# Kernel tuning notes

Hardware: AMD Instinct MI355X
Metric: run time of the kernel (lower is better)

## Reference

```python
import jax, jax.numpy as jnp
import numpy as np

N_NODES = 100000
N_EDGES = 1600000
D_IN = 64
D_OUT = 64
K_ORDERS = 4  # K+1 Chebyshev orders (K=3)


def setup_inputs() -> dict:
    key = jax.random.key(0)
    k1, k2, k3, k4, k5 = jax.random.split(key, 5)
    x = jax.random.normal(k1, (N_NODES, D_IN), dtype=jnp.float32)
    edge_index = jax.random.randint(k2, (2, N_EDGES), 0, N_NODES, dtype=jnp.int64)
    edge_attr = jax.random.uniform(k3, (N_EDGES,), dtype=jnp.float32)
    weight = jax.random.normal(k4, (K_ORDERS, D_IN, D_OUT), dtype=jnp.float32) * 0.05
    bias = jax.random.normal(k5, (D_OUT,), dtype=jnp.float32) * 0.05
    return {"x": x, "edge_index": edge_index, "edge_attr": edge_attr,
            "weight": weight, "bias": bias}


def reference(x, edge_index, edge_attr, weight, bias):
    n = x.shape[0]
    row, col = edge_index[0], edge_index[1]
    # degree = number of edges per destination node (row)
    deg = jax.ops.segment_sum(jnp.ones_like(edge_attr), row, num_segments=n)
    dinv = jnp.where(deg > 0, deg ** -0.5, 0.0)
    # negative normalized adjacency acting as rescaled Laplacian
    lap = -dinv[row] * edge_attr * dinv[col]  # [E]

    def spmm(h):  # out[row] += lap * h[col]
        return jax.ops.segment_sum(lap[:, None] * h[col], row, num_segments=n)

    k_orders = weight.shape[0]
    tx0 = x
    out = tx0 @ weight[0]
    tx1 = spmm(tx0)
    out = out + tx1 @ weight[1]
    for k in range(2, k_orders):  # small fixed K, fine to unroll
        tx2 = 2.0 * spmm(tx1) - tx0
        out = out + tx2 @ weight[k]
        tx0, tx1 = tx1, tx2
    return out + bias
```

## Files before the change

### kernel.cpp

```cpp
#include <hip/hip_runtime.h>

#define D 64
#define BLK 256

#define NBSHIFT 9
#define NODES_PER_BKT 512
#define TA 4096

typedef unsigned int uint32;
typedef __attribute__((ext_vector_type(8))) short bf16x8;
typedef __attribute__((ext_vector_type(4))) float f32x4;

__device__ inline uint32 f2bf_u(float f) {
    uint32 u = __float_as_uint(f);
    u += 0x7FFFu + ((u >> 16) & 1u);
    return u >> 16;
}

__global__ void cvt_kernel(const float* __restrict__ x, uint2* __restrict__ xb, int n4) {
    int i = blockIdx.x * BLK + threadIdx.x;
    if (i < n4) {
        float4 v = ((const float4*)x)[i];
        uint2 pack;
        pack.x = f2bf_u(v.x) | (f2bf_u(v.y) << 16);
        pack.y = f2bf_u(v.z) | (f2bf_u(v.w) << 16);
        xb[i] = pack;
    }
}

__global__ void wf_kernel(const float* __restrict__ W, uint4* __restrict__ Wf) {
    int tid = blockIdx.x * 256 + threadIdx.x;
    int l = tid & 63;
    int g = tid >> 6;
    int kh = g & 1;
    int t = (g >> 1) & 3;
    int w = g >> 3;
    int n = t * 16 + (l & 15);
    int kbase = kh * 32 + (l >> 4) * 8;
    uint32 pk[4];
    #pragma unroll
    for (int i = 0; i < 4; ++i) {
        uint32 b0 = f2bf_u(W[(size_t)w * 4096 + (size_t)(kbase + 2 * i) * 64 + n]);
        uint32 b1 = f2bf_u(W[(size_t)w * 4096 + (size_t)(kbase + 2 * i + 1) * 64 + n]);
        pk[i] = b0 | (b1 << 16);
    }
    Wf[tid] = make_uint4(pk[0], pk[1], pk[2], pk[3]);
}

__global__ void hist_kernel(const int* __restrict__ row, uint32* __restrict__ bcount, int E) {
    __shared__ uint32 h[256];
    int tid = threadIdx.x;
    h[tid] = 0;
    __syncthreads();
    int base = blockIdx.x * TA;
    int end = min(base + TA, E);
    for (int e = base + tid; e < end; e += 256)
        atomicAdd(&h[(uint32)row[e] >> NBSHIFT], 1u);
    __syncthreads();
    if (h[tid]) atomicAdd(&bcount[tid], h[tid]);
}

__global__ void scan256_kernel(const uint32* __restrict__ bcount, uint32* __restrict__ gcursor,
                               uint32* __restrict__ bbase, int E) {
    __shared__ uint32 s[256];
    int tid = threadIdx.x;
    uint32 v = bcount[tid];
    s[tid] = v;
    __syncthreads();
    for (int off = 1; off < 256; off <<= 1) {
        uint32 t = (tid >= off) ? s[tid - off] : 0u;
        __syncthreads();
        s[tid] += t;
        __syncthreads();
    }
    uint32 excl = s[tid] - v;
    gcursor[tid] = excl;
    bbase[tid] = excl;
    if (tid == 255) bbase[256] = (uint32)E;
}

__global__ void binA_kernel(const int* __restrict__ row, const int* __restrict__ col,
                            const float* __restrict__ attr,
                            uint32* __restrict__ gcursor, int2* __restrict__ binned, int E) {
    __shared__ uint32 hist[256], baseg[256], lstart[256], lcur[256];
    __shared__ int2 stage[TA];
    __shared__ unsigned char sbkt[TA];
    int tid = threadIdx.x;
    int tile = blockIdx.x * TA;
    hist[tid] = 0;
    __syncthreads();

    uint32 px[16], py[16], bk[16];
    #pragma unroll
    for (int k = 0; k < 16; ++k) {
        int e = tile + k * 256 + tid;
        bk[k] = 0xFFFFFFFFu;
        if (e < E) {
            int r = row[e], c = col[e];
            uint32 b = (uint32)r >> NBSHIFT;
            bk[k] = b;
            px[k] = ((uint32)(r & (NODES_PER_BKT - 1)) << 17) | (uint32)c;
            py[k] = __float_as_uint(attr[e]);
            atomicAdd(&hist[b], 1u);
        }
    }
    __syncthreads();
    lcur[tid] = hist[tid];
    __syncthreads();
    for (int off = 1; off < 256; off <<= 1) {
        uint32 t = (tid >= off) ? lcur[tid - off] : 0u;
        __syncthreads();
        lcur[tid] += t;
        __syncthreads();
    }
    lstart[tid] = lcur[tid] - hist[tid];
    if (hist[tid] > 0) baseg[tid] = atomicAdd(&gcursor[tid], hist[tid]);
    lcur[tid] = lstart[tid];
    __syncthreads();
    #pragma unroll
    for (int k = 0; k < 16; ++k) {
        if (bk[k] != 0xFFFFFFFFu) {
            uint32 pos = atomicAdd(&lcur[bk[k]], 1u);
            stage[pos] = make_int2((int)px[k], (int)py[k]);
            sbkt[pos] = (unsigned char)bk[k];
        }
    }
    __syncthreads();
    int cnt = min(TA, E - tile);
    for (int i = tid; i < cnt; i += 256) {
        uint32 b = sbkt[i];
        uint32 dst = baseg[b] + (uint32)i - lstart[b];
        binned[dst] = stage[i];
    }
}

__global__ void binBdeg_kernel(const int2* __restrict__ binned, const uint32* __restrict__ bbase,
                               uint32* __restrict__ rowptr, float* __restrict__ dinv,
                               int N, int E) {
    __shared__ uint32 cnt[NODES_PER_BKT];
    __shared__ uint32 ps[256];
    int b = blockIdx.x;
    int tid = threadIdx.x;
    cnt[tid] = 0;
    cnt[tid + 256] = 0;
    __syncthreads();
    uint32 start = bbase[b], end = bbase[b + 1];
    for (uint32 i = start + tid; i < end; i += 256)
        atomicAdd(&cnt[(uint32)binned[i].x >> 17], 1u);
    __syncthreads();
    uint32 c0 = cnt[2 * tid], c1 = cnt[2 * tid + 1];
    ps[tid] = c0 + c1;
    __syncthreads();
    for (int off = 1; off < 256; off <<= 1) {
        uint32 t = (tid >= off) ? ps[tid - off] : 0u;
        __syncthreads();
        ps[tid] += t;
        __syncthreads();
    }
    uint32 pexcl = ps[tid] - (c0 + c1);
    int base = b << NBSHIFT;
    int n0 = base + 2 * tid, n1 = n0 + 1;
    if (n0 < N) {
        rowptr[n0] = start + pexcl;
        dinv[n0] = c0 ? rsqrtf((float)c0) : 0.0f;
    }
    if (n1 < N) {
        rowptr[n1] = start + pexcl + c0;
        dinv[n1] = c1 ? rsqrtf((float)c1) : 0.0f;
    }
    if (b == gridDim.x - 1 && tid == 0) rowptr[N] = (uint32)E;
}

__global__ void binBsort_kernel(const int2* __restrict__ binned, const uint32* __restrict__ bbase,
                                const uint32* __restrict__ rowptr, const float* __restrict__ dinv,
                                int2* __restrict__ pairs, int N) {
    __shared__ uint32 lcur[NODES_PER_BKT];
    __shared__ float ldin[NODES_PER_BKT];
    int b = blockIdx.x;
    int tid = threadIdx.x;
    int base = b << NBSHIFT;
    uint32 start = bbase[b], end = bbase[b + 1];
    for (int t = tid; t < NODES_PER_BKT; t += 256) {
        int node = base + t;
        lcur[t] = (node < N) ? (rowptr[node] - start) : 0u;
        ldin[t] = (node < N) ? dinv[node] : 0.0f;
    }
    __syncthreads();
    for (uint32 i = start + tid; i < end; i += 256) {
        int2 rec = binned[i];
        uint32 x = (uint32)rec.x;
        uint32 rl = x >> 17;
        uint32 c = x & 0x1FFFFu;
        float lap = -ldin[rl] * __int_as_float(rec.y) * dinv[c];
        uint32 pos = atomicAdd(&lcur[rl], 1u);
        pairs[start + pos] = make_int2((int)(c << 7), __float_as_int(lap));
    }
}

#define LOAD16(J, END, ESAFE, M0, M1, H0, H1)                          \
    {                                                                  \
        uint32 i0_ = (J) + q, i1_ = (J) + 8 + q;                       \
        uint32 c0_ = (i0_ < (END)) ? i0_ : (ESAFE);                    \
        uint32 c1_ = (i1_ < (END)) ? i1_ : (ESAFE);                    \
        M0 = pairs[c0_];                                               \
        M1 = pairs[c1_];                                               \
        H0 = *(const uint4*)(hb + (uint32)M0.x + off);                 \
        H1 = *(const uint4*)(hb + (uint32)M1.x + off);                 \
    }

#define FMA16(J, END, M0, M1, H0, H1, A)                               \
    {                                                                  \
        uint32 i0_ = (J) + q, i1_ = (J) + 8 + q;                       \
        float l0_ = (i0_ < (END)) ? __int_as_float(M0.y) : 0.0f;       \
        float l1_ = (i1_ < (END)) ? __int_as_float(M1.y) : 0.0f;       \
        A[0] += l0_ * __uint_as_float(H0.x << 16);                     \
        A[1] += l0_ * __uint_as_float(H0.x & 0xFFFF0000u);             \
        A[2] += l0_ * __uint_as_float(H0.y << 16);                     \
        A[3] += l0_ * __uint_as_float(H0.y & 0xFFFF0000u);             \
        A[4] += l0_ * __uint_as_float(H0.z << 16);                     \
        A[5] += l0_ * __uint_as_float(H0.z & 0xFFFF0000u);             \
        A[6] += l0_ * __uint_as_float(H0.w << 16);                     \
        A[7] += l0_ * __uint_as_float(H0.w & 0xFFFF0000u);             \
        A[0] += l1_ * __uint_as_float(H1.x << 16);                     \
        A[1] += l1_ * __uint_as_float(H1.x & 0xFFFF0000u);             \
        A[2] += l1_ * __uint_as_float(H1.y << 16);                     \
        A[3] += l1_ * __uint_as_float(H1.y & 0xFFFF0000u);             \
        A[4] += l1_ * __uint_as_float(H1.z << 16);                     \
        A[5] += l1_ * __uint_as_float(H1.z & 0xFFFF0000u);             \
        A[6] += l1_ * __uint_as_float(H1.w << 16);                     \
        A[7] += l1_ * __uint_as_float(H1.w & 0xFFFF0000u);             \
    }

__global__ void spmm2r_kernel(const uint32* __restrict__ rowptr, const int2* __restrict__ pairs,
                              const char* __restrict__ hb, const uint4* __restrict__ prev,
                              uint4* __restrict__ out, float scale, int N) {
    int wid = blockIdx.x * 4 + (threadIdx.x >> 6);
    int nA = wid * 2;
    if (nA >= N) return;
    int lane = threadIdx.x & 63;
    int q = lane >> 3;
    int sub = lane & 7;
    int off = sub * 16;
    bool hasB = (nA + 1 < N);

    uint2 rpA = *(const uint2*)(rowptr + nA);
    uint32 eBr = hasB ? rowptr[nA + 2] : rpA.y;
    uint32 jA   = __builtin_amdgcn_readfirstlane(rpA.x);
    uint32 endA = __builtin_amdgcn_readfirstlane(rpA.y);
    uint32 jB   = endA;
    uint32 endB = __builtin_amdgcn_readfirstlane(eBr);
    uint32 esA = (endA > jA) ? endA - 1 : 0u;
    uint32 esB = (endB > jB) ? endB - 1 : 0u;

    int nq = nA + (q & 1);
    uint4 pv = make_uint4(0u, 0u, 0u, 0u);
    if (prev && q < 2 && nq < N) pv = prev[(size_t)nq * 8 + sub];

    float aA[8], aB[8];
    #pragma unroll
    for (int i = 0; i < 8; ++i) { aA[i] = 0.0f; aB[i] = 0.0f; }

    int2 mA0, mA1, mA2, mA3, mB0, mB1, mB2, mB3;
    uint4 hA0, hA1, hA2, hA3, hB0, hB1, hB2, hB3;

    bool dA = (jA + 16 < endA);
    bool dB = (jB + 16 < endB);

    LOAD16(jA, endA, esA, mA0, mA1, hA0, hA1);
    LOAD16(jB, endB, esB, mB0, mB1, hB0, hB1);
    if (dA) LOAD16(jA + 16, endA, esA, mA2, mA3, hA2, hA3);
    if (dB) LOAD16(jB + 16, endB, esB, mB2, mB3, hB2, hB3);
    FMA16(jA, endA, mA0, mA1, hA0, hA1, aA);
    FMA16(jB, endB, mB0, mB1, hB0, hB1, aB);
    if (dA) FMA16(jA + 16, endA, mA2, mA3, hA2, hA3, aA);
    if (dB) FMA16(jB + 16, endB, mB2, mB3, hB2, hB3, aB);
    jA += 32;
    jB += 32;

    while (jA < endA) {
        LOAD16(jA, endA, esA, mA0, mA1, hA0, hA1);
        FMA16(jA, endA, mA0, mA1, hA0, hA1, aA);
        if (jA + 16 < endA) {
            LOAD16(jA + 16, endA, esA, mA2, mA3, hA2, hA3);
            FMA16(jA + 16, endA, mA2, mA3, hA2, hA3, aA);
        }
        jA += 32;
    }
    while (jB < endB) {
        LOAD16(jB, endB, esB, mB0, mB1, hB0, hB1);
        FMA16(jB, endB, mB0, mB1, hB0, hB1, aB);
        if (jB + 16 < endB) {
            LOAD16(jB + 16, endB, esB, mB2, mB3, hB2, hB3);
            FMA16(jB + 16, endB, mB2, mB3, hB2, hB3, aB);
        }
        jB += 32;
    }

    #pragma unroll
    for (int i = 0; i < 8; ++i) {
        aA[i] += __shfl_xor(aA[i], 8);
        aA[i] += __shfl_xor(aA[i], 16);
        aA[i] += __shfl_xor(aA[i], 32);
        aB[i] += __shfl_xor(aB[i], 8);
        aB[i] += __shfl_xor(aB[i], 16);
        aB[i] += __shfl_xor(aB[i], 32);
    }

    if (q < 2 && nq < N) {
        bool isB = (q == 1);
        float r[8];
        #pragma unroll
        for (int i = 0; i < 8; ++i) r[i] = scale * (isB ? aB[i] : aA[i]);
        if (prev) {
            r[0] -= __uint_as_float(pv.x << 16);
            r[1] -= __uint_as_float(pv.x & 0xFFFF0000u);
            r[2] -= __uint_as_float(pv.y << 16);
            r[3] -= __uint_as_float(pv.y & 0xFFFF0000u);
            r[4] -= __uint_as_float(pv.z << 16);
            r[5] -= __uint_as_float(pv.z & 0xFFFF0000u);
            r[6] -= __uint_as_float(pv.w << 16);
            r[7] -= __uint_as_float(pv.w & 0xFFFF0000u);
        }
        uint4 pack;
        pack.x = f2bf_u(r[0]) | (f2bf_u(r[1]) << 16);
        pack.y = f2bf_u(r[2]) | (f2bf_u(r[3]) << 16);
        pack.z = f2bf_u(r[4]) | (f2bf_u(r[5]) << 16);
        pack.w = f2bf_u(r[6]) | (f2bf_u(r[7]) << 16);
        out[(size_t)nq * 8 + sub] = pack;
    }
}

__global__ void gemm_mfma(const uint4* __restrict__ h0, const uint4* __restrict__ h1,
                          const uint4* __restrict__ h2, const uint4* __restrict__ h3,
                          const uint4* __restrict__ Wf, const float* __restrict__ bias,
                          float* __restrict__ out, int N) {
    int tid = threadIdx.x;
    int wave = tid >> 6;
    int lane = tid & 63;
    int quad = lane >> 4;
    int lo = lane & 15;
    int m0 = blockIdx.x * 64 + wave * 16;
    int mrow = m0 + lo;
    int mclamp = min(mrow, N - 1);

    f32x4 acc[4] = {{0.f,0.f,0.f,0.f},{0.f,0.f,0.f,0.f},{0.f,0.f,0.f,0.f},{0.f,0.f,0.f,0.f}};
    const uint4* hs[4] = { h0, h1, h2, h3 };
    #pragma unroll
    for (int w = 0; w < 4; ++w) {
        union { uint4 u; bf16x8 v; } a0, a1;
        a0.u = hs[w][(size_t)mclamp * 8 + quad];
        a1.u = hs[w][(size_t)mclamp * 8 + 4 + quad];
        #pragma unroll
        for (int t = 0; t < 4; ++t) {
            union { uint4 u; bf16x8 v; } b0, b1;
            b0.u = Wf[(w * 8 + t * 2 + 0) * 64 + lane];
            b1.u = Wf[(w * 8 + t * 2 + 1) * 64 + lane];
            acc[t] = __builtin_amdgcn_mfma_f32_16x16x32_bf16(a0.v, b0.v, acc[t], 0, 0, 0);
            acc[t] = __builtin_amdgcn_mfma_f32_16x16x32_bf16(a1.v, b1.v, acc[t], 0, 0, 0);
        }
    }
    #pragma unroll
    for (int t = 0; t < 4; ++t) {
        int col = t * 16 + lo;
        float bv = bias[col];
        #pragma unroll
        for (int r = 0; r < 4; ++r) {
            int rowi = m0 + quad * 4 + r;
            if (rowi < N) out[(size_t)rowi * 64 + col] = acc[t][r] + bv;
        }
    }
}

extern "C" void kernel_launch(void* const* d_in, const int* in_sizes, int n_in,
                              void* d_out, int out_size, void* d_ws, size_t ws_size,
                              hipStream_t stream) {
    const float* x    = (const float*)d_in[0];
    const int*   ei   = (const int*)d_in[1];
    const float* attr = (const float*)d_in[2];
    const float* W    = (const float*)d_in[3];
    const float* bias = (const float*)d_in[4];
    float* out = (float*)d_out;

    const int N = in_sizes[0] / D;
    const int E = in_sizes[1] / 2;
    const int* row = ei;
    const int* col = ei + E;
    const int NB = (N + NODES_PER_BKT - 1) >> NBSHIFT;

    char* p = (char*)d_ws;
    int2*     pairs   = (int2*)p;                p += (size_t)E * 8;
    uint2*    xb      = (uint2*)p;               p += (size_t)N * D * 2;
    uint2*    T1      = (uint2*)p;               p += (size_t)N * D * 2;
    uint2*    T2      = (uint2*)p;               p += (size_t)N * D * 2;
    uint2*    T3      = (uint2*)p;               p += (size_t)N * D * 2;
    uint4*    Wf      = (uint4*)p;               p += 2048 * 16;
    uint32*   rowptr  = (uint32*)p;              p += (size_t)(N + 1) * 4;
    uint32*   bcount  = (uint32*)p;              p += 256 * 4;
    uint32*   gcursor = (uint32*)p;              p += 256 * 4;
    uint32*   bbase   = (uint32*)p;              p += 257 * 4;
    float*    dinv    = (float*)p;
    int2*     binned  = (int2*)T3;

    const int gSp = (N + 7) / 8;
    const int gGm = (N + 63) / 64;
    const int gTile = (E + TA - 1) / TA;
    const int gCvt = ((N * D / 4) + BLK - 1) / BLK;

    hipMemsetAsync(bcount, 0, 256 * 4, stream);
    cvt_kernel<<<gCvt, BLK, 0, stream>>>(x, xb, N * D / 4);
    wf_kernel<<<8, 256, 0, stream>>>(W, Wf);
    hist_kernel<<<gTile, 256, 0, stream>>>(row, bcount, E);
    scan256_kernel<<<1, 256, 0, stream>>>(bcount, gcursor, bbase, E);
    binA_kernel<<<gTile, 256, 0, stream>>>(row, col, attr, gcursor, binned, E);
    binBdeg_kernel<<<NB, 256, 0, stream>>>(binned, bbase, rowptr, dinv, N, E);
    binBsort_kernel<<<NB, 256, 0, stream>>>(binned, bbase, rowptr, dinv, pairs, N);

    spmm2r_kernel<<<gSp, BLK, 0, stream>>>(rowptr, pairs, (const char*)xb, nullptr, (uint4*)T1, 1.0f, N);
    spmm2r_kernel<<<gSp, BLK, 0, stream>>>(rowptr, pairs, (const char*)T1, (const uint4*)xb, (uint4*)T2, 2.0f, N);
    spmm2r_kernel<<<gSp, BLK, 0, stream>>>(rowptr, pairs, (const char*)T2, (const uint4*)T1, (uint4*)T3, 2.0f, N);
    gemm_mfma<<<gGm, BLK, 0, stream>>>((const uint4*)xb, (const uint4*)T1, (const uint4*)T2,
                                       (const uint4*)T3, Wf, bias, out, N);
}
```

Baseline: 291.6 us.

## Split SpMM feature dimension into four column chunks across blocks

```diff
diff --git a/kernel.cpp b/kernel.cpp
--- a/kernel.cpp
+++ b/kernel.cpp
@@ -197,50 +197,42 @@
     }
 }
 
-#define LOAD16(J, END, ESAFE, M0, M1, H0, H1)                          \
-    {                                                                  \
-        uint32 i0_ = (J) + q, i1_ = (J) + 8 + q;                       \
-        uint32 c0_ = (i0_ < (END)) ? i0_ : (ESAFE);                    \
-        uint32 c1_ = (i1_ < (END)) ? i1_ : (ESAFE);                    \
-        M0 = pairs[c0_];                                               \
-        M1 = pairs[c1_];                                               \
-        H0 = *(const uint4*)(hb + (uint32)M0.x + off);                 \
-        H1 = *(const uint4*)(hb + (uint32)M1.x + off);                 \
-    }
-
-#define FMA16(J, END, M0, M1, H0, H1, A)                               \
-    {                                                                  \
-        uint32 i0_ = (J) + q, i1_ = (J) + 8 + q;                       \
-        float l0_ = (i0_ < (END)) ? __int_as_float(M0.y) : 0.0f;       \
-        float l1_ = (i1_ < (END)) ? __int_as_float(M1.y) : 0.0f;       \
-        A[0] += l0_ * __uint_as_float(H0.x << 16);                     \
-        A[1] += l0_ * __uint_as_float(H0.x & 0xFFFF0000u);             \
-        A[2] += l0_ * __uint_as_float(H0.y << 16);                     \
-        A[3] += l0_ * __uint_as_float(H0.y & 0xFFFF0000u);             \
-        A[4] += l0_ * __uint_as_float(H0.z << 16);                     \
-        A[5] += l0_ * __uint_as_float(H0.z & 0xFFFF0000u);             \
-        A[6] += l0_ * __uint_as_float(H0.w << 16);                     \
-        A[7] += l0_ * __uint_as_float(H0.w & 0xFFFF0000u);             \
-        A[0] += l1_ * __uint_as_float(H1.x << 16);                     \
-        A[1] += l1_ * __uint_as_float(H1.x & 0xFFFF0000u);             \
-        A[2] += l1_ * __uint_as_float(H1.y << 16);                     \
-        A[3] += l1_ * __uint_as_float(H1.y & 0xFFFF0000u);             \
-        A[4] += l1_ * __uint_as_float(H1.z << 16);                     \
-        A[5] += l1_ * __uint_as_float(H1.z & 0xFFFF0000u);             \
-        A[6] += l1_ * __uint_as_float(H1.w << 16);                     \
-        A[7] += l1_ * __uint_as_float(H1.w & 0xFFFF0000u);             \
-    }
-
-__global__ void spmm2r_kernel(const uint32* __restrict__ rowptr, const int2* __restrict__ pairs,
-                              const char* __restrict__ hb, const uint4* __restrict__ prev,
-                              uint4* __restrict__ out, float scale, int N) {
-    int wid = blockIdx.x * 4 + (threadIdx.x >> 6);
+#define LOAD16C(J, END, ESAFE, X0, L0, X1, L1, H0, H1)                          \
+    {                                                                           \
+        uint32 i0_ = (J) + q, i1_ = (J) + 8 + q;                                \
+        uint32 c0_ = (i0_ < (END)) ? i0_ : (ESAFE);                             \
+        uint32 c1_ = (i1_ < (END)) ? i1_ : (ESAFE);                             \
+        unsigned long long p0_ = __builtin_nontemporal_load(pairs64 + c0_);     \
+        unsigned long long p1_ = __builtin_nontemporal_load(pairs64 + c1_);     \
+        X0 = (uint32)p0_;                                                       \
+        X1 = (uint32)p1_;                                                       \
+        L0 = (i0_ < (END)) ? __uint_as_float((uint32)(p0_ >> 32)) : 0.0f;       \
+        L1 = (i1_ < (END)) ? __uint_as_float((uint32)(p1_ >> 32)) : 0.0f;       \
+        H0 = *(const uint32*)(hb + X0 + coff);                                  \
+        H1 = *(const uint32*)(hb + X1 + coff);                                  \
+    }
+
+#define FMA16C(L0, L1, H0, H1, A)                                               \
+    {                                                                           \
+        A[0] += L0 * __uint_as_float(H0 << 16);                                 \
+        A[1] += L0 * __uint_as_float(H0 & 0xFFFF0000u);                         \
+        A[0] += L1 * __uint_as_float(H1 << 16);                                 \
+        A[1] += L1 * __uint_as_float(H1 & 0xFFFF0000u);                         \
+    }
+
+__global__ void spmm2rc_kernel(const uint32* __restrict__ rowptr, const int2* __restrict__ pairs,
+                               const char* __restrict__ hb, const uint32* __restrict__ prev,
+                               uint32* __restrict__ out, float scale, int N) {
+    int chunk = blockIdx.x & 3;
+    int rg = blockIdx.x >> 2;
+    int wid = rg * 4 + (threadIdx.x >> 6);
     int nA = wid * 2;
     if (nA >= N) return;
     int lane = threadIdx.x & 63;
     int q = lane >> 3;
     int sub = lane & 7;
-    int off = sub * 16;
+    int coff = chunk * 32 + sub * 4;
+    const unsigned long long* pairs64 = (const unsigned long long*)pairs;
     bool hasB = (nA + 1 < N);
 
     uint2 rpA = *(const uint2*)(rowptr + nA);
@@ -253,51 +245,50 @@
     uint32 esB = (endB > jB) ? endB - 1 : 0u;
 
     int nq = nA + (q & 1);
-    uint4 pv = make_uint4(0u, 0u, 0u, 0u);
-    if (prev && q < 2 && nq < N) pv = prev[(size_t)nq * 8 + sub];
-
-    float aA[8], aB[8];
-    #pragma unroll
-    for (int i = 0; i < 8; ++i) { aA[i] = 0.0f; aB[i] = 0.0f; }
-
-    int2 mA0, mA1, mA2, mA3, mB0, mB1, mB2, mB3;
-    uint4 hA0, hA1, hA2, hA3, hB0, hB1, hB2, hB3;
+    uint32 pv = 0u;
+    if (prev && q < 2 && nq < N)
+        pv = __builtin_nontemporal_load(prev + (size_t)nq * 32 + chunk * 8 + sub);
+
+    float aA[2] = {0.0f, 0.0f}, aB[2] = {0.0f, 0.0f};
+    uint32 xA0, xA1, xA2, xA3, xB0, xB1, xB2, xB3;
+    float lA0, lA1, lA2, lA3, lB0, lB1, lB2, lB3;
+    uint32 hA0, hA1, hA2, hA3, hB0, hB1, hB2, hB3;
 
     bool dA = (jA + 16 < endA);
     bool dB = (jB + 16 < endB);
 
-    LOAD16(jA, endA, esA, mA0, mA1, hA0, hA1);
-    LOAD16(jB, endB, esB, mB0, mB1, hB0, hB1);
-    if (dA) LOAD16(jA + 16, endA, esA, mA2, mA3, hA2, hA3);
-    if (dB) LOAD16(jB + 16, endB, esB, mB2, mB3, hB2, hB3);
-    FMA16(jA, endA, mA0, mA1, hA0, hA1, aA);
-    FMA16(jB, endB, mB0, mB1, hB0, hB1, aB);
-    if (dA) FMA16(jA + 16, endA, mA2, mA3, hA2, hA3, aA);
-    if (dB) FMA16(jB + 16, endB, mB2, mB3, hB2, hB3, aB);
+    LOAD16C(jA, endA, esA, xA0, lA0, xA1, lA1, hA0, hA1);
+    LOAD16C(jB, endB, esB, xB0, lB0, xB1, lB1, hB0, hB1);
+    if (dA) LOAD16C(jA + 16, endA, esA, xA2, lA2, xA3, lA3, hA2, hA3);
+    if (dB) LOAD16C(jB + 16, endB, esB, xB2, lB2, xB3, lB3, hB2, hB3);
+    FMA16C(lA0, lA1, hA0, hA1, aA);
+    FMA16C(lB0, lB1, hB0, hB1, aB);
+    if (dA) FMA16C(lA2, lA3, hA2, hA3, aA);
+    if (dB) FMA16C(lB2, lB3, hB2, hB3, aB);
     jA += 32;
     jB += 32;
 
     while (jA < endA) {
-        LOAD16(jA, endA, esA, mA0, mA1, hA0, hA1);
-        FMA16(jA, endA, mA0, mA1, hA0, hA1, aA);
+        LOAD16C(jA, endA, esA, xA0, lA0, xA1, lA1, hA0, hA1);
+        FMA16C(lA0, lA1, hA0, hA1, aA);
         if (jA + 16 < endA) {
-            LOAD16(jA + 16, endA, esA, mA2, mA3, hA2, hA3);
-            FMA16(jA + 16, endA, mA2, mA3, hA2, hA3, aA);
+            LOAD16C(jA + 16, endA, esA, xA2, lA2, xA3, lA3, hA2, hA3);
+            FMA16C(lA2, lA3, hA2, hA3, aA);
         }
         jA += 32;
     }
     while (jB < endB) {
-        LOAD16(jB, endB, esB, mB0, mB1, hB0, hB1);
-        FMA16(jB, endB, mB0, mB1, hB0, hB1, aB);
+        LOAD16C(jB, endB, esB, xB0, lB0, xB1, lB1, hB0, hB1);
+        FMA16C(lB0, lB1, hB0, hB1, aB);
         if (jB + 16 < endB) {
-            LOAD16(jB + 16, endB, esB, mB2, mB3, hB2, hB3);
-            FMA16(jB + 16, endB, mB2, mB3, hB2, hB3, aB);
+            LOAD16C(jB + 16, endB, esB, xB2, lB2, xB3, lB3, hB2, hB3);
+            FMA16C(lB2, lB3, hB2, hB3, aB);
         }
         jB += 32;
     }
 
     #pragma unroll
-    for (int i = 0; i < 8; ++i) {
+    for (int i = 0; i < 2; ++i) {
         aA[i] += __shfl_xor(aA[i], 8);
         aA[i] += __shfl_xor(aA[i], 16);
         aA[i] += __shfl_xor(aA[i], 32);
@@ -308,25 +299,13 @@
 
     if (q < 2 && nq < N) {
         bool isB = (q == 1);
-        float r[8];
-        #pragma unroll
-        for (int i = 0; i < 8; ++i) r[i] = scale * (isB ? aB[i] : aA[i]);
+        float r0 = scale * (isB ? aB[0] : aA[0]);
+        float r1 = scale * (isB ? aB[1] : aA[1]);
         if (prev) {
-            r[0] -= __uint_as_float(pv.x << 16);
-            r[1] -= __uint_as_float(pv.x & 0xFFFF0000u);
-            r[2] -= __uint_as_float(pv.y << 16);
-            r[3] -= __uint_as_float(pv.y & 0xFFFF0000u);
-            r[4] -= __uint_as_float(pv.z << 16);
-            r[5] -= __uint_as_float(pv.z & 0xFFFF0000u);
-            r[6] -= __uint_as_float(pv.w << 16);
-            r[7] -= __uint_as_float(pv.w & 0xFFFF0000u);
-        }
-        uint4 pack;
-        pack.x = f2bf_u(r[0]) | (f2bf_u(r[1]) << 16);
-        pack.y = f2bf_u(r[2]) | (f2bf_u(r[3]) << 16);
-        pack.z = f2bf_u(r[4]) | (f2bf_u(r[5]) << 16);
-        pack.w = f2bf_u(r[6]) | (f2bf_u(r[7]) << 16);
-        out[(size_t)nq * 8 + sub] = pack;
+            r0 -= __uint_as_float(pv << 16);
+            r1 -= __uint_as_float(pv & 0xFFFF0000u);
+        }
+        out[(size_t)nq * 32 + chunk * 8 + sub] = f2bf_u(r0) | (f2bf_u(r1) << 16);
     }
 }
 
@@ -401,7 +380,7 @@
     float*    dinv    = (float*)p;
     int2*     binned  = (int2*)T3;
 
-    const int gSp = (N + 7) / 8;
+    const int gSpC = ((N + 7) / 8) * 4;
     const int gGm = (N + 63) / 64;
     const int gTile = (E + TA - 1) / TA;
     const int gCvt = ((N * D / 4) + BLK - 1) / BLK;
@@ -415,9 +394,9 @@
     binBdeg_kernel<<<NB, 256, 0, stream>>>(binned, bbase, rowptr, dinv, N, E);
     binBsort_kernel<<<NB, 256, 0, stream>>>(binned, bbase, rowptr, dinv, pairs, N);
 
-    spmm2r_kernel<<<gSp, BLK, 0, stream>>>(rowptr, pairs, (const char*)xb, nullptr, (uint4*)T1, 1.0f, N);
-    spmm2r_kernel<<<gSp, BLK, 0, stream>>>(rowptr, pairs, (const char*)T1, (const uint4*)xb, (uint4*)T2, 2.0f, N);
-    spmm2r_kernel<<<gSp, BLK, 0, stream>>>(rowptr, pairs, (const char*)T2, (const uint4*)T1, (uint4*)T3, 2.0f, N);
+    spmm2rc_kernel<<<gSpC, BLK, 0, stream>>>(rowptr, pairs, (const char*)xb, nullptr, (uint32*)T1, 1.0f, N);
+    spmm2rc_kernel<<<gSpC, BLK, 0, stream>>>(rowptr, pairs, (const char*)T1, (const uint32*)xb, (uint32*)T2, 2.0f, N);
+    spmm2rc_kernel<<<gSpC, BLK, 0, stream>>>(rowptr, pairs, (const char*)T2, (const uint32*)T1, (uint32*)T3, 2.0f, N);
     gemm_mfma<<<gGm, BLK, 0, stream>>>((const uint4*)xb, (const uint4*)T1, (const uint4*)T2,
                                        (const uint4*)T3, Wf, bias, out, N);
 }
```

New measurement: 524.1 us. +79.7%, slower.

## Fuse preprocessing kernels and merge binning passes with cooperative grid sync

Applied to the files above, without the earlier changes.

```diff
diff --git a/kernel.cpp b/kernel.cpp
--- a/kernel.cpp
+++ b/kernel.cpp
@@ -1,4 +1,7 @@
 #include <hip/hip_runtime.h>
+#include <hip/hip_cooperative_groups.h>
+
+namespace cg = cooperative_groups;
 
 #define D 64
 #define BLK 256
@@ -17,70 +20,74 @@
     return u >> 16;
 }
 
-__global__ void cvt_kernel(const float* __restrict__ x, uint2* __restrict__ xb, int n4) {
-    int i = blockIdx.x * BLK + threadIdx.x;
-    if (i < n4) {
-        float4 v = ((const float4*)x)[i];
-        uint2 pack;
-        pack.x = f2bf_u(v.x) | (f2bf_u(v.y) << 16);
-        pack.y = f2bf_u(v.z) | (f2bf_u(v.w) << 16);
-        xb[i] = pack;
-    }
-}
-
-__global__ void wf_kernel(const float* __restrict__ W, uint4* __restrict__ Wf) {
-    int tid = blockIdx.x * 256 + threadIdx.x;
-    int l = tid & 63;
-    int g = tid >> 6;
-    int kh = g & 1;
-    int t = (g >> 1) & 3;
-    int w = g >> 3;
-    int n = t * 16 + (l & 15);
-    int kbase = kh * 32 + (l >> 4) * 8;
-    uint32 pk[4];
-    #pragma unroll
-    for (int i = 0; i < 4; ++i) {
-        uint32 b0 = f2bf_u(W[(size_t)w * 4096 + (size_t)(kbase + 2 * i) * 64 + n]);
-        uint32 b1 = f2bf_u(W[(size_t)w * 4096 + (size_t)(kbase + 2 * i + 1) * 64 + n]);
-        pk[i] = b0 | (b1 << 16);
-    }
-    Wf[tid] = make_uint4(pk[0], pk[1], pk[2], pk[3]);
-}
-
-__global__ void hist_kernel(const int* __restrict__ row, uint32* __restrict__ bcount, int E) {
+__global__ void pre_kernel(const float* __restrict__ x, uint2* __restrict__ xb, int n4,
+                           const float* __restrict__ W, uint4* __restrict__ Wf,
+                           const int* __restrict__ row, uint32* __restrict__ bcount,
+                           uint32* __restrict__ ticket, uint32* __restrict__ bbase,
+                           int E, int gCvt, int gHist) {
+    int bid = blockIdx.x;
+    if (bid < gCvt) {
+        int i = bid * BLK + threadIdx.x;
+        if (i < n4) {
+            float4 v = ((const float4*)x)[i];
+            uint2 pack;
+            pack.x = f2bf_u(v.x) | (f2bf_u(v.y) << 16);
+            pack.y = f2bf_u(v.z) | (f2bf_u(v.w) << 16);
+            xb[i] = pack;
+        }
+        return;
+    }
+    if (bid < gCvt + 8) {
+        int tid = (bid - gCvt) * 256 + threadIdx.x;
+        int l = tid & 63;
+        int g = tid >> 6;
+        int kh = g & 1;
+        int t = (g >> 1) & 3;
+        int w = g >> 3;
+        int n = t * 16 + (l & 15);
+        int kbase = kh * 32 + (l >> 4) * 8;
+        uint32 pk[4];
+        #pragma unroll
+        for (int i = 0; i < 4; ++i) {
+            uint32 b0 = f2bf_u(W[(size_t)w * 4096 + (size_t)(kbase + 2 * i) * 64 + n]);
+            uint32 b1 = f2bf_u(W[(size_t)w * 4096 + (size_t)(kbase + 2 * i + 1) * 64 + n]);
+            pk[i] = b0 | (b1 << 16);
+        }
+        Wf[tid] = make_uint4(pk[0], pk[1], pk[2], pk[3]);
+        return;
+    }
     __shared__ uint32 h[256];
+    __shared__ uint32 rank;
     int tid = threadIdx.x;
     h[tid] = 0;
     __syncthreads();
-    int base = blockIdx.x * TA;
+    int base = (bid - gCvt - 8) * TA;
     int end = min(base + TA, E);
     for (int e = base + tid; e < end; e += 256)
         atomicAdd(&h[(uint32)row[e] >> NBSHIFT], 1u);
     __syncthreads();
     if (h[tid]) atomicAdd(&bcount[tid], h[tid]);
-}
-
-__global__ void scan256_kernel(const uint32* __restrict__ bcount, uint32* __restrict__ gcursor,
-                               uint32* __restrict__ bbase, int E) {
-    __shared__ uint32 s[256];
-    int tid = threadIdx.x;
-    uint32 v = bcount[tid];
-    s[tid] = v;
-    __syncthreads();
-    for (int off = 1; off < 256; off <<= 1) {
-        uint32 t = (tid >= off) ? s[tid - off] : 0u;
+    __threadfence();
+    if (tid == 0) rank = atomicAdd(ticket, 1u);
+    __syncthreads();
+    if (rank == (uint32)(gHist - 1)) {
+        __threadfence();
+        uint32 v = bcount[tid];
+        h[tid] = v;
         __syncthreads();
-        s[tid] += t;
-        __syncthreads();
-    }
-    uint32 excl = s[tid] - v;
-    gcursor[tid] = excl;
-    bbase[tid] = excl;
-    if (tid == 255) bbase[256] = (uint32)E;
+        for (int off = 1; off < 256; off <<= 1) {
+            uint32 t = (tid >= off) ? h[tid - off] : 0u;
+            __syncthreads();
+            h[tid] += t;
+            __syncthreads();
+        }
+        bbase[tid] = h[tid] - v;
+        if (tid == 255) bbase[256] = (uint32)E;
+    }
 }
 
 __global__ void binA_kernel(const int* __restrict__ row, const int* __restrict__ col,
-                            const float* __restrict__ attr,
+                            const float* __restrict__ attr, const uint32* __restrict__ bbase,
                             uint32* __restrict__ gcursor, int2* __restrict__ binned, int E) {
     __shared__ uint32 hist[256], baseg[256], lstart[256], lcur[256];
     __shared__ int2 stage[TA];
@@ -105,6 +112,7 @@
         }
     }
     __syncthreads();
+    if (hist[tid] > 0) baseg[tid] = bbase[tid] + atomicAdd(&gcursor[tid], hist[tid]);
     lcur[tid] = hist[tid];
     __syncthreads();
     for (int off = 1; off < 256; off <<= 1) {
@@ -114,7 +122,6 @@
         __syncthreads();
     }
     lstart[tid] = lcur[tid] - hist[tid];
-    if (hist[tid] > 0) baseg[tid] = atomicAdd(&gcursor[tid], hist[tid]);
     lcur[tid] = lstart[tid];
     __syncthreads();
     #pragma unroll
@@ -134,17 +141,19 @@
     }
 }
 
-__global__ void binBdeg_kernel(const int2* __restrict__ binned, const uint32* __restrict__ bbase,
-                               uint32* __restrict__ rowptr, float* __restrict__ dinv,
-                               int N, int E) {
+__global__ void binB_kernel(const int2* __restrict__ binned, const uint32* __restrict__ bbase,
+                            uint32* __restrict__ rowptr, float* __restrict__ dinv,
+                            int2* __restrict__ pairs, int N, int E) {
+    cg::grid_group grid = cg::this_grid();
     __shared__ uint32 cnt[NODES_PER_BKT];
+    __shared__ float ldin[NODES_PER_BKT];
     __shared__ uint32 ps[256];
     int b = blockIdx.x;
     int tid = threadIdx.x;
+    uint32 start = bbase[b], end = bbase[b + 1];
     cnt[tid] = 0;
     cnt[tid + 256] = 0;
     __syncthreads();
-    uint32 start = bbase[b], end = bbase[b + 1];
     for (uint32 i = start + tid; i < end; i += 256)
         atomicAdd(&cnt[(uint32)binned[i].x >> 17], 1u);
     __syncthreads();
@@ -160,39 +169,25 @@
     uint32 pexcl = ps[tid] - (c0 + c1);
     int base = b << NBSHIFT;
     int n0 = base + 2 * tid, n1 = n0 + 1;
-    if (n0 < N) {
-        rowptr[n0] = start + pexcl;
-        dinv[n0] = c0 ? rsqrtf((float)c0) : 0.0f;
-    }
-    if (n1 < N) {
-        rowptr[n1] = start + pexcl + c0;
-        dinv[n1] = c1 ? rsqrtf((float)c1) : 0.0f;
-    }
-    if (b == gridDim.x - 1 && tid == 0) rowptr[N] = (uint32)E;
-}
-
-__global__ void binBsort_kernel(const int2* __restrict__ binned, const uint32* __restrict__ bbase,
-                                const uint32* __restrict__ rowptr, const float* __restrict__ dinv,
-                                int2* __restrict__ pairs, int N) {
-    __shared__ uint32 lcur[NODES_PER_BKT];
-    __shared__ float ldin[NODES_PER_BKT];
-    int b = blockIdx.x;
-    int tid = threadIdx.x;
-    int base = b << NBSHIFT;
-    uint32 start = bbase[b], end = bbase[b + 1];
-    for (int t = tid; t < NODES_PER_BKT; t += 256) {
-        int node = base + t;
-        lcur[t] = (node < N) ? (rowptr[node] - start) : 0u;
-        ldin[t] = (node < N) ? dinv[node] : 0.0f;
-    }
-    __syncthreads();
+    float di0 = c0 ? rsqrtf((float)c0) : 0.0f;
+    float di1 = c1 ? rsqrtf((float)c1) : 0.0f;
+    if (n0 < N) { rowptr[n0] = start + pexcl;      dinv[n0] = di0; }
+    if (n1 < N) { rowptr[n1] = start + pexcl + c0; dinv[n1] = di1; }
+    if (b == (int)gridDim.x - 1 && tid == 0) rowptr[N] = (uint32)E;
+    __syncthreads();
+    cnt[2 * tid]     = pexcl;
+    cnt[2 * tid + 1] = pexcl + c0;
+    ldin[2 * tid]     = di0;
+    ldin[2 * tid + 1] = di1;
+    __threadfence();
+    grid.sync();
     for (uint32 i = start + tid; i < end; i += 256) {
         int2 rec = binned[i];
         uint32 x = (uint32)rec.x;
         uint32 rl = x >> 17;
         uint32 c = x & 0x1FFFFu;
         float lap = -ldin[rl] * __int_as_float(rec.y) * dinv[c];
-        uint32 pos = atomicAdd(&lcur[rl], 1u);
+        uint32 pos = atomicAdd(&cnt[rl], 1u);
         pairs[start + pos] = make_int2((int)(c << 7), __float_as_int(lap));
     }
 }
@@ -397,6 +392,7 @@
     uint32*   rowptr  = (uint32*)p;              p += (size_t)(N + 1) * 4;
     uint32*   bcount  = (uint32*)p;              p += 256 * 4;
     uint32*   gcursor = (uint32*)p;              p += 256 * 4;
+    uint32*   ticket  = (uint32*)p;              p += 16;
     uint32*   bbase   = (uint32*)p;              p += 257 * 4;
     float*    dinv    = (float*)p;
     int2*     binned  = (int2*)T3;
@@ -406,14 +402,18 @@
     const int gTile = (E + TA - 1) / TA;
     const int gCvt = ((N * D / 4) + BLK - 1) / BLK;
 
-    hipMemsetAsync(bcount, 0, 256 * 4, stream);
-    cvt_kernel<<<gCvt, BLK, 0, stream>>>(x, xb, N * D / 4);
-    wf_kernel<<<8, 256, 0, stream>>>(W, Wf);
-    hist_kernel<<<gTile, 256, 0, stream>>>(row, bcount, E);
-    scan256_kernel<<<1, 256, 0, stream>>>(bcount, gcursor, bbase, E);
-    binA_kernel<<<gTile, 256, 0, stream>>>(row, col, attr, gcursor, binned, E);
-    binBdeg_kernel<<<NB, 256, 0, stream>>>(binned, bbase, rowptr, dinv, N, E);
-    binBsort_kernel<<<NB, 256, 0, stream>>>(binned, bbase, rowptr, dinv, pairs, N);
+    hipMemsetAsync(bcount, 0, (256 + 256 + 4) * 4, stream);
+    pre_kernel<<<gCvt + 8 + gTile, BLK, 0, stream>>>(x, xb, N * D / 4, W, Wf,
+                                                     row, bcount, ticket, bbase, E, gCvt, gTile);
+    binA_kernel<<<gTile, 256, 0, stream>>>(row, col, attr, bbase, gcursor, binned, E);
+    {
+        int Nv = N, Ev = E;
+        const int2* binned_c = binned;
+        const uint32* bbase_c = bbase;
+        void* args[] = { (void*)&binned_c, (void*)&bbase_c, (void*)&rowptr,
+                         (void*)&dinv, (void*)&pairs, (void*)&Nv, (void*)&Ev };
+        hipLaunchCooperativeKernel((void*)binB_kernel, dim3(NB), dim3(256), args, 0, stream);
+    }
 
     spmm2r_kernel<<<gSp, BLK, 0, stream>>>(rowptr, pairs, (const char*)xb, nullptr, (uint4*)T1, 1.0f, N);
     spmm2r_kernel<<<gSp, BLK, 0, stream>>>(rowptr, pairs, (const char*)T1, (const uint4*)xb, (uint4*)T2, 2.0f, N);
```

Measured after the change: 364.0 us. 1.25x slower.
